# Performance work log

Hardware: AMD Instinct MI355X
Metric: run time of the kernel (lower is better)

The kernel has to match this reference:

```python
import jax, jax.numpy as jnp
import numpy as np

N_REGIONS = 20000
N_EMB = 5
N_INT = 5

def setup_inputs() -> dict:
    key = jax.random.key(0)
    k1, k2, k3, k4, k5, k6 = jax.random.split(key, 6)
    cell_region_embedding = jax.random.normal(k1, (4096, 4096, N_EMB), dtype=jnp.float32)
    region_ix = jax.random.randint(k2, (4096,), 0, N_REGIONS, dtype=jnp.int64)
    # per-region parameter tables (original inits to 0; randn for meaningful test)
    weight1 = jax.random.normal(k3, (N_REGIONS, N_EMB, N_INT), dtype=jnp.float32) * 0.1
    bias1 = jax.random.normal(k4, (N_REGIONS, N_INT), dtype=jnp.float32) * 0.1
    weight2 = jax.random.normal(k5, (N_REGIONS, N_INT, 1), dtype=jnp.float32) * 0.1
    bias2 = jax.random.normal(k6, (N_REGIONS, 1), dtype=jnp.float32) * 0.1
    return {
        "cell_region_embedding": cell_region_embedding,
        "region_ix": region_ix,
        "weight1": weight1,
        "bias1": bias1,
        "weight2": weight2,
        "bias2": bias2,
    }

def reference(cell_region_embedding, region_ix, weight1, bias1, weight2, bias2):
    # gather per-region params: [b, c, d] and [b, d]
    w1 = weight1[region_ix]   # [regions_b, n_emb, n_int]
    b1 = bias1[region_ix]     # [regions_b, n_int]
    w2 = weight2[region_ix]   # [regions_b, n_int, 1]
    b2 = bias2[region_ix]     # [regions_b, 1]
    # linear1 + sigmoid: [cells, regions_b, n_int]
    h = jax.nn.sigmoid(jnp.einsum('abc,bcd->abd', cell_region_embedding, w1) + b1)
    # linear2, squeeze last dim: [cells, regions_b]
    out = (jnp.einsum('abc,bcd->abd', h, w2) + b2).squeeze(-1)
    return out
```

## Files before the change

kernel.cpp:

```cpp
#include <hip/hip_runtime.h>
#include <hip/hip_bf16.h>


#define NA 4096
#define NB 4096
#define NE 5
#define NI 5
#define ROWS 32
#define SROWS 4
#define ROW_FLOATS (256 * NE)

__global__ __launch_bounds__(256) void e2e_kernel(
    const float* __restrict__ E,
    const int*   __restrict__ rix,
    const float* __restrict__ w1,
    const float* __restrict__ b1,
    const float* __restrict__ w2,
    const float* __restrict__ b2,
    float*       __restrict__ out)
{
    __shared__ float lds[SROWS * ROW_FLOATS];

    const int tid  = threadIdx.x;
    const int b0   = blockIdx.x * 256;
    const int b    = b0 + tid;
    const int a0   = blockIdx.y * ROWS;
    const int srow = tid >> 6;
    const int lane = tid & 63;

    const int r = rix[b];

    float W1[NE][NI];
    const float* w1p = w1 + (size_t)r * (NE * NI);
#pragma unroll
    for (int c = 0; c < NE; ++c)
#pragma unroll
        for (int d = 0; d < NI; ++d)
            W1[c][d] = w1p[c * NI + d];

    float B1[NI], W2[NI];
    const float* b1p = b1 + (size_t)r * NI;
    const float* w2p = w2 + (size_t)r * NI;
#pragma unroll
    for (int d = 0; d < NI; ++d) {
        B1[d] = b1p[d];
        W2[d] = w2p[d];
    }
    const float B2 = b2[r];

#pragma unroll 1
    for (int chunk = 0; chunk < ROWS / SROWS; ++chunk) {
        const int a_ld = a0 + chunk * SROWS + srow;
        const float4* src = (const float4*)(E + ((size_t)a_ld * NB + b0) * NE);
        float4* dst = (float4*)(lds + srow * ROW_FLOATS);
#pragma unroll
        for (int j = 0; j < ROW_FLOATS / 4 / 64; ++j)
            dst[lane + j * 64] = src[lane + j * 64];

        __syncthreads();

#pragma unroll
        for (int s = 0; s < SROWS; ++s) {
            const float* e = lds + s * ROW_FLOATS + tid * NE;
            const float e0 = e[0], e1 = e[1], e2 = e[2], e3 = e[3], e4 = e[4];

            float acc = B2;
#pragma unroll
            for (int d = 0; d < NI; ++d) {
                float h = B1[d]
                        + e0 * W1[0][d]
                        + e1 * W1[1][d]
                        + e2 * W1[2][d]
                        + e3 * W1[3][d]
                        + e4 * W1[4][d];
                h = 1.0f / (1.0f + __expf(-h));
                acc += h * W2[d];
            }
            out[(size_t)(a0 + chunk * SROWS + s) * NB + b] = acc;
        }

        __syncthreads();
    }
}

extern "C" void kernel_launch(void* const* d_in, const int* in_sizes, int n_in,
                              void* d_out, int out_size, void* d_ws, size_t ws_size,
                              hipStream_t stream) {
    const float* E   = (const float*)d_in[0];
    const int*   rix = (const int*)  d_in[1];
    const float* w1  = (const float*)d_in[2];
    const float* b1  = (const float*)d_in[3];
    const float* w2  = (const float*)d_in[4];
    const float* b2  = (const float*)d_in[5];
    float*       out = (float*)d_out;

    dim3 grid(NB / 256, NA / ROWS);
    dim3 block(256);
    hipLaunchKernelGGL(e2e_kernel, grid, block, 0, stream, E, rix, w1, b1, w2, b2, out);
}
```

Measured before the change: 477.1 us.

## Prefetch next embedding chunk into registers and pre-pack gathered region params

Adds a small pre-kernel that gathers the per-region parameters into a column-major packed workspace, so the main kernel loads them with coalesced accesses instead of scattered gathers. The main kernel now software-pipelines the embedding tile: the next chunk is loaded into registers while the current one is computed from LDS. The sigmoid also switches to a hardware reciprocal. This costs an extra kernel launch and more register pressure, and the packed path only runs if a large enough workspace is supplied.

```diff
diff --git a/kernel.cpp b/kernel.cpp
--- a/kernel.cpp
+++ b/kernel.cpp
@@ -1,17 +1,44 @@
 #include <hip/hip_runtime.h>
-#include <hip/hip_bf16.h>
 
 
 #define NA 4096
 #define NB 4096
 #define NE 5
 #define NI 5
+#define NPAR 36
 #define ROWS 32
 #define SROWS 4
 #define ROW_FLOATS (256 * NE)
+#define NCHUNK (ROWS / SROWS)
 
+__global__ __launch_bounds__(256) void pack_params(
+    const int*   __restrict__ rix,
+    const float* __restrict__ w1,
+    const float* __restrict__ b1,
+    const float* __restrict__ w2,
+    const float* __restrict__ b2,
+    float*       __restrict__ pk)
+{
+    const int b = blockIdx.x * 256 + threadIdx.x;
+    const int r = rix[b];
+    const float* w1p = w1 + (size_t)r * (NE * NI);
+    const float* b1p = b1 + (size_t)r * NI;
+    const float* w2p = w2 + (size_t)r * NI;
+#pragma unroll
+    for (int j = 0; j < NE * NI; ++j)
+        pk[(size_t)j * NB + b] = w1p[j];
+#pragma unroll
+    for (int d = 0; d < NI; ++d) {
+        pk[(size_t)(25 + d) * NB + b] = b1p[d];
+        pk[(size_t)(30 + d) * NB + b] = w2p[d];
+    }
+    pk[(size_t)35 * NB + b] = b2[r];
+}
+
+template <bool PK>
 __global__ __launch_bounds__(256) void e2e_kernel(
     const float* __restrict__ E,
+    const float* __restrict__ pk,
     const int*   __restrict__ rix,
     const float* __restrict__ w1,
     const float* __restrict__ b1,
@@ -28,55 +55,71 @@
     const int srow = tid >> 6;
     const int lane = tid & 63;
 
-    const int r = rix[b];
+    float4 pf0, pf1, pf2, pf3, pf4;
+    {
+        const float4* src = (const float4*)(E + (((size_t)a0 + srow) * NB + b0) * NE);
+        pf0 = src[lane];
+        pf1 = src[lane + 64];
+        pf2 = src[lane + 128];
+        pf3 = src[lane + 192];
+        pf4 = src[lane + 256];
+    }
 
-    float W1[NE][NI];
-    const float* w1p = w1 + (size_t)r * (NE * NI);
+    float P[NPAR];
+    if (PK) {
 #pragma unroll
-    for (int c = 0; c < NE; ++c)
+        for (int j = 0; j < NPAR; ++j)
+            P[j] = pk[(size_t)j * NB + b];
+    } else {
+        const int r = rix[b];
+        const float* w1p = w1 + (size_t)r * (NE * NI);
+        const float* b1p = b1 + (size_t)r * NI;
+        const float* w2p = w2 + (size_t)r * NI;
 #pragma unroll
-        for (int d = 0; d < NI; ++d)
-            W1[c][d] = w1p[c * NI + d];
-
-    float B1[NI], W2[NI];
-    const float* b1p = b1 + (size_t)r * NI;
-    const float* w2p = w2 + (size_t)r * NI;
+        for (int j = 0; j < NE * NI; ++j) P[j] = w1p[j];
 #pragma unroll
-    for (int d = 0; d < NI; ++d) {
-        B1[d] = b1p[d];
-        W2[d] = w2p[d];
+        for (int d = 0; d < NI; ++d) { P[25 + d] = b1p[d]; P[30 + d] = w2p[d]; }
+        P[35] = b2[r];
     }
-    const float B2 = b2[r];
 
 #pragma unroll 1
-    for (int chunk = 0; chunk < ROWS / SROWS; ++chunk) {
-        const int a_ld = a0 + chunk * SROWS + srow;
-        const float4* src = (const float4*)(E + ((size_t)a_ld * NB + b0) * NE);
+    for (int chunk = 0; chunk < NCHUNK; ++chunk) {
         float4* dst = (float4*)(lds + srow * ROW_FLOATS);
-#pragma unroll
-        for (int j = 0; j < ROW_FLOATS / 4 / 64; ++j)
-            dst[lane + j * 64] = src[lane + j * 64];
+        dst[lane]       = pf0;
+        dst[lane + 64]  = pf1;
+        dst[lane + 128] = pf2;
+        dst[lane + 192] = pf3;
+        dst[lane + 256] = pf4;
+        __syncthreads();
 
-        __syncthreads();
+        if (chunk + 1 < NCHUNK) {
+            const float4* src = (const float4*)(
+                E + (((size_t)a0 + (chunk + 1) * SROWS + srow) * NB + b0) * NE);
+            pf0 = src[lane];
+            pf1 = src[lane + 64];
+            pf2 = src[lane + 128];
+            pf3 = src[lane + 192];
+            pf4 = src[lane + 256];
+        }
 
 #pragma unroll
         for (int s = 0; s < SROWS; ++s) {
             const float* e = lds + s * ROW_FLOATS + tid * NE;
             const float e0 = e[0], e1 = e[1], e2 = e[2], e3 = e[3], e4 = e[4];
 
-            float acc = B2;
+            float acc = P[35];
 #pragma unroll
             for (int d = 0; d < NI; ++d) {
-                float h = B1[d]
-                        + e0 * W1[0][d]
-                        + e1 * W1[1][d]
-                        + e2 * W1[2][d]
-                        + e3 * W1[3][d]
-                        + e4 * W1[4][d];
-                h = 1.0f / (1.0f + __expf(-h));
-                acc += h * W2[d];
+                float h = P[25 + d]
+                        + e0 * P[d]
+                        + e1 * P[5 + d]
+                        + e2 * P[10 + d]
+                        + e3 * P[15 + d]
+                        + e4 * P[20 + d];
+                const float sg = __builtin_amdgcn_rcpf(1.0f + __expf(-h));
+                acc = fmaf(sg, P[30 + d], acc);
             }
-            out[(size_t)(a0 + chunk * SROWS + s) * NB + b] = acc;
+            out[((size_t)(a0 + chunk * SROWS + s)) * NB + b] = acc;
         }
 
         __syncthreads();
@@ -96,5 +139,16 @@
 
     dim3 grid(NB / 256, NA / ROWS);
     dim3 block(256);
-    hipLaunchKernelGGL(e2e_kernel, grid, block, 0, stream, E, rix, w1, b1, w2, b2, out);
+
+    const size_t pk_bytes = (size_t)NPAR * NB * sizeof(float);
+    if (d_ws != nullptr && ws_size >= pk_bytes) {
+        float* pk = (float*)d_ws;
+        hipLaunchKernelGGL(pack_params, dim3(NB / 256), block, 0, stream,
+                           rix, w1, b1, w2, b2, pk);
+        hipLaunchKernelGGL((e2e_kernel<true>), grid, block, 0, stream,
+                           E, pk, rix, w1, b1, w2, b2, out);
+    } else {
+        hipLaunchKernelGGL((e2e_kernel<false>), grid, block, 0, stream,
+                           E, nullptr, rix, w1, b1, w2, b2, out);
+    }
 }
```

Result: no change. 479.7 us (+0.6%).
